# Performance work log

Measured on AMD Instinct MI355X. Metric: run time of the kernel, lower is better.

## Reference

```python
import jax, jax.numpy as jnp
import numpy as np

B, S, D, H, DH = 2, 4096, 1024, 8, 128
BLK, TOPK = 512, 4
NBLK = S // BLK
EPS = 1e-5
NEG = -1e9


def _rope_tables():
    pos = np.arange(S, dtype=np.float32)
    inv = 1.0 / (10000.0 ** (np.arange(0, DH, 2, dtype=np.float32) / DH))
    ang = pos[:, None] * inv[None, :]              # [S, DH/2]
    cos = np.concatenate([np.cos(ang), np.cos(ang)], axis=-1)  # [S, DH]
    sin = np.concatenate([np.sin(ang), np.sin(ang)], axis=-1)
    return jnp.asarray(cos), jnp.asarray(sin)


def setup_inputs() -> dict:
    key = jax.random.key(0)
    ks = jax.random.split(key, 8)
    sc = 0.02
    cos, sin = _rope_tables()
    return {
        "hidden_states": jax.random.normal(ks[0], (B, S, D), jnp.float32),
        "ln1_w": jnp.ones((D,), jnp.float32), "ln1_b": jnp.zeros((D,), jnp.float32),
        "wq": jax.random.normal(ks[1], (D, D), jnp.float32) * sc, "bq": jnp.zeros((D,), jnp.float32),
        "wk": jax.random.normal(ks[2], (D, D), jnp.float32) * sc, "bk": jnp.zeros((D,), jnp.float32),
        "wv": jax.random.normal(ks[3], (D, D), jnp.float32) * sc, "bv": jnp.zeros((D,), jnp.float32),
        "wo": jax.random.normal(ks[4], (D, D), jnp.float32) * sc, "bo": jnp.zeros((D,), jnp.float32),
        "ln2_w": jnp.ones((D,), jnp.float32), "ln2_b": jnp.zeros((D,), jnp.float32),
        "wi": jax.random.normal(ks[5], (D, 4 * D), jnp.float32) * sc, "bi": jnp.zeros((4 * D,), jnp.float32),
        "wo2": jax.random.normal(ks[6], (4 * D, D), jnp.float32) * sc, "bo2": jnp.zeros((D,), jnp.float32),
        "cos": cos, "sin": sin,
    }


def _ln(x, w, b):
    mu = x.mean(-1, keepdims=True)
    var = ((x - mu) ** 2).mean(-1, keepdims=True)
    return (x - mu) * jax.lax.rsqrt(var + EPS) * w + b


def _rotate_half(x):
    x1, x2 = jnp.split(x, 2, axis=-1)
    return jnp.concatenate([-x2, x1], axis=-1)


def _moba_attn(x, wq, bq, wk, bk, wv, bv, wo, bo, cos, sin):
    # projections -> [B, H, S, DH]
    def heads(t):
        return t.reshape(B, S, H, DH).transpose(0, 2, 1, 3)
    q = heads(x @ wq + bq)
    k = heads(x @ wk + bk)
    v = heads(x @ wv + bv)
    c = cos[None, None]; s = sin[None, None]
    q = q * c + _rotate_half(q) * s
    k = k * c + _rotate_half(k) * s
    scale = 1.0 / jnp.sqrt(jnp.asarray(DH, q.dtype))

    # block routing: mean-pooled keys per block -> gate scores [B,H,S,NBLK]
    kmean = k.reshape(B, H, NBLK, BLK, DH).mean(axis=3)
    gate = jnp.einsum("bhsd,bhnd->bhsn", q, kmean) * scale
    pos = jnp.arange(S)
    blk_start = jnp.arange(NBLK) * BLK
    visible = blk_start[None, :] <= pos[:, None]            # [S, NBLK] block has >=1 causal key
    gate = jnp.where(visible[None, None], gate, NEG)
    _, top_idx = jax.lax.top_k(gate, TOPK)                  # [B,H,S,TOPK]
    sel = jax.nn.one_hot(top_idx, NBLK, dtype=jnp.float32).sum(-2)  # [B,H,S,NBLK]
    cur = jax.nn.one_hot(pos // BLK, NBLK, dtype=jnp.float32)       # always attend own block
    sel_blocks = (sel + cur[None, None]) > 0
    sel_keys = jnp.repeat(sel_blocks, BLK, axis=-1)          # [B,H,S,S]

    scores = jnp.einsum("bhid,bhjd->bhij", q, k) * scale
    causal = pos[None, :] <= pos[:, None]
    mask = sel_keys & causal[None, None]
    scores = jnp.where(mask, scores, NEG)
    probs = jax.nn.softmax(scores, axis=-1)
    out = jnp.einsum("bhij,bhjd->bhid", probs, v)
    out = out.transpose(0, 2, 1, 3).reshape(B, S, D)
    return out @ wo + bo


def reference(hidden_states, ln1_w, ln1_b, wq, bq, wk, bk, wv, bv, wo, bo,
              ln2_w, ln2_b, wi, bi, wo2, bo2, cos, sin):
    residual = hidden_states
    x = _ln(hidden_states, ln1_w, ln1_b)
    x = residual + _moba_attn(x, wq, bq, wk, bk, wv, bv, wo, bo, cos, sin)
    residual = x
    h = _ln(x, ln2_w, ln2_b)
    h = jax.nn.gelu(h @ wi + bi, approximate=False)
    h = h @ wo2 + bo2
    return residual + h
```

## Files before the change

### kernel.cpp

```cpp
#include <hip/hip_runtime.h>
#include <cstdint>

#define S_LEN 4096
#define NHEAD 8
#define DHEAD 128
#define DMODEL 1024
#define MOBA_TOPK 4

typedef __attribute__((ext_vector_type(8))) short short8;
typedef __attribute__((ext_vector_type(4))) float f32x4;

__device__ inline float bf2f(short s) {
  return __builtin_bit_cast(float, (unsigned)((unsigned short)s) << 16);
}
__device__ inline short f2bf(float f) {
  unsigned u = __builtin_bit_cast(unsigned, f);
  unsigned r = (u + 0x7fffu + ((u >> 16) & 1u)) >> 16;
  return (short)(unsigned short)r;
}
__device__ inline float toF(float v) { return v; }
__device__ inline float toF(short v) { return bf2f(v); }

#define MFMA(a, b, c) __builtin_amdgcn_mfma_f32_16x16x32_bf16(a, b, c, 0, 0, 0)
#define GLOAD_LDS(gsrc, ldst)                                                  \
  __builtin_amdgcn_global_load_lds(                                            \
      (const __attribute__((address_space(1))) void*)(gsrc),                   \
      (__attribute__((address_space(3))) void*)(ldst), 16, 0, 0)

template <typename T>
__global__ __launch_bounds__(256) void transpose_bf16(const T* __restrict__ in,
                                                      short* __restrict__ out,
                                                      int R, int C) {
  __shared__ float tile[32][33];
  size_t bo = (size_t)blockIdx.z * R * C;
  int c0 = blockIdx.x * 32, r0 = blockIdx.y * 32;
  int tx = threadIdx.x & 31, ty = threadIdx.x >> 5;
#pragma unroll
  for (int i = 0; i < 32; i += 8)
    tile[ty + i][tx] = toF(in[bo + (size_t)(r0 + ty + i) * C + c0 + tx]);
  __syncthreads();
#pragma unroll
  for (int i = 0; i < 32; i += 8)
    out[bo + (size_t)(c0 + ty + i) * R + r0 + tx] = f2bf(tile[tx][ty + i]);
}

__global__ __launch_bounds__(256) void pack_bias(const float* __restrict__ bq,
                                                 const float* __restrict__ bk,
                                                 const float* __restrict__ bv,
                                                 float* __restrict__ dst) {
  int i = blockIdx.x * 256 + threadIdx.x;
  const float* src = (i < 1024) ? bq : (i < 2048) ? bk : bv;
  dst[i] = src[i & 1023];
}

__global__ __launch_bounds__(256) void ln_kernel(const float* __restrict__ x,
                                                 const float* __restrict__ w,
                                                 const float* __restrict__ b,
                                                 short* __restrict__ out) {
  int row = blockIdx.x * 4 + (threadIdx.x >> 6);
  int lane = threadIdx.x & 63;
  const float* xr = x + (size_t)row * DMODEL + lane * 16;
  f32x4 v[4];
  float sum = 0.f, sq = 0.f;
#pragma unroll
  for (int i = 0; i < 4; ++i) {
    v[i] = *(const f32x4*)(xr + i * 4);
#pragma unroll
    for (int j = 0; j < 4; ++j) {
      sum += v[i][j];
      sq += v[i][j] * v[i][j];
    }
  }
#pragma unroll
  for (int d = 1; d < 64; d <<= 1) {
    sum += __shfl_xor(sum, d, 64);
    sq += __shfl_xor(sq, d, 64);
  }
  float mu = sum * (1.f / DMODEL);
  float var = sq * (1.f / DMODEL) - mu * mu;
  float rstd = rsqrtf(var + 1e-5f);
  short* orow = out + (size_t)row * DMODEL;
#pragma unroll
  for (int i = 0; i < 4; ++i)
#pragma unroll
    for (int j = 0; j < 4; ++j) {
      int c = lane * 16 + i * 4 + j;
      orow[c] = f2bf((v[i][j] - mu) * rstd * w[c] + b[c]);
    }
}

template <int BN, int WM, int MODE>
__global__ __launch_bounds__(512, 2) void gemm256(const short* __restrict__ A,
                                                  const short* __restrict__ BT,
                                                  const float* __restrict__ bias,
                                                  const float* __restrict__ residF,
                                                  short* __restrict__ outB,
                                                  float* outF, int M, int N,
                                                  int K) {
  constexpr int MF = 16 / WM;
  constexpr int NWN = 8 / WM;
  constexpr int RB = BN / 64;
  __shared__ alignas(16) short As[2][16384];
  __shared__ alignas(16) short Bs[2][BN * 64];

  const int t = threadIdx.x, lane = t & 63, w = t >> 6;
  const int wm = w / NWN, wn = w % NWN;
  const int m0 = blockIdx.y * 256, n0 = blockIdx.x * BN;
  const int wmBase = wm * (256 / WM);
  const int wnBase = wn * 64;
  const int lr = lane & 15;
  const int koff0 = ((((lane >> 4) << 4)) ^ ((lane & 7) << 4)) >> 1;
  const int koff1 = ((64 + ((lane >> 4) << 4)) ^ ((lane & 7) << 4)) >> 1;

  const f32x4 fz = {0.f, 0.f, 0.f, 0.f};
  f32x4 acc[MF][4];
#pragma unroll
  for (int i = 0; i < MF; ++i)
#pragma unroll
    for (int j = 0; j < 4; ++j) acc[i][j] = fz;

  auto stageA = [&](short* dst, int k0) {
#pragma unroll
    for (int rd = 0; rd < 4; ++rd) {
      int p = (t << 4) + (rd << 13);
      int row = p >> 7;
      int ks = ((p & 127) ^ ((row & 7) << 4)) >> 1;
      GLOAD_LDS(A + (size_t)(m0 + row) * K + k0 + ks, dst + (p >> 1));
    }
  };
  auto stageB = [&](short* dst, int k0) {
#pragma unroll
    for (int rd = 0; rd < RB; ++rd) {
      int p = (t << 4) + (rd << 13);
      int row = p >> 7;
      int ks = ((p & 127) ^ ((row & 7) << 4)) >> 1;
      GLOAD_LDS(BT + (size_t)(n0 + row) * K + k0 + ks, dst + (p >> 1));
    }
  };

  const int NT = K >> 6;
  stageA(&As[0][0], 0);
  stageB(&Bs[0][0], 0);
  __syncthreads();

  for (int kt = 0; kt < NT; ++kt) {
    const int cur = kt & 1;
    if (kt + 1 < NT) {
      stageA(&As[cur ^ 1][0], (kt + 1) << 6);
      stageB(&Bs[cur ^ 1][0], (kt + 1) << 6);
    }
    __builtin_amdgcn_sched_barrier(0);
    short8 bfr[4][2];
#pragma unroll
    for (int ni = 0; ni < 4; ++ni) {
      int rb = (wnBase + ni * 16 + lr) << 6;
      bfr[ni][0] = *(const short8*)(&Bs[cur][rb + koff0]);
      bfr[ni][1] = *(const short8*)(&Bs[cur][rb + koff1]);
    }
#pragma unroll
    for (int pp = 0; pp < MF / 2; ++pp) {
      const int ra0 = (wmBase + (pp * 2) * 16 + lr) << 6;
      const int ra1 = (wmBase + (pp * 2 + 1) * 16 + lr) << 6;
      short8 a00 = *(const short8*)(&As[cur][ra0 + koff0]);
      short8 a01 = *(const short8*)(&As[cur][ra0 + koff1]);
      short8 a10 = *(const short8*)(&As[cur][ra1 + koff0]);
      short8 a11 = *(const short8*)(&As[cur][ra1 + koff1]);
      __builtin_amdgcn_sched_barrier(0);
      __builtin_amdgcn_s_setprio(1);
#pragma unroll
      for (int ni = 0; ni < 4; ++ni) {
        acc[pp * 2][ni] = MFMA(a00, bfr[ni][0], acc[pp * 2][ni]);
        acc[pp * 2][ni] = MFMA(a01, bfr[ni][1], acc[pp * 2][ni]);
        acc[pp * 2 + 1][ni] = MFMA(a10, bfr[ni][0], acc[pp * 2 + 1][ni]);
        acc[pp * 2 + 1][ni] = MFMA(a11, bfr[ni][1], acc[pp * 2 + 1][ni]);
      }
      __builtin_amdgcn_s_setprio(0);
      __builtin_amdgcn_sched_barrier(0);
    }
    __syncthreads();
  }

  const int er = lane >> 4, ec = lane & 15;
#pragma unroll
  for (int mi = 0; mi < MF; ++mi) {
#pragma unroll
    for (int ni = 0; ni < 4; ++ni) {
      int col = n0 + wnBase + ni * 16 + ec;
      float bs = bias[col];
#pragma unroll
      for (int r = 0; r < 4; ++r) {
        int row = m0 + wmBase + mi * 16 + er * 4 + r;
        float v = acc[mi][ni][r] + bs;
        size_t idx = (size_t)row * N + col;
        if (MODE == 1) {
          v += residF[idx];
          outF[idx] = v;
        } else if (MODE == 2) {
          float gl = 0.5f * v * (1.f + erff(v * 0.70710678118654752f));
          outB[idx] = f2bf(gl);
        } else if (MODE == 3) {
          v += outF[idx];
          outF[idx] = v;
        } else {
          int b = row >> 12, s = row & 4095;
          int tens = col >> 10, rem = col & 1023;
          int h = rem >> 7, dh = rem & 127;
          outB[(size_t)tens * 8388608 +
               ((size_t)((b * NHEAD + h) * S_LEN + s)) * DHEAD + dh] = f2bf(v);
        }
      }
    }
  }
}

__global__ __launch_bounds__(256) void rope_kernel(short* __restrict__ q,
                                                   short* __restrict__ k,
                                                   const float* __restrict__ cosT,
                                                   const float* __restrict__ sinT) {
  int row = blockIdx.x * 4 + (threadIdx.x >> 6);
  int lane = threadIdx.x & 63;
  int s = row & (S_LEN - 1);
  float c1 = cosT[s * DHEAD + lane], s1 = sinT[s * DHEAD + lane];
  float c2 = cosT[s * DHEAD + 64 + lane], s2 = sinT[s * DHEAD + 64 + lane];
  size_t base = (size_t)row * DHEAD;
  float a = bf2f(q[base + lane]), bb = bf2f(q[base + 64 + lane]);
  q[base + lane] = f2bf(a * c1 - bb * s1);
  q[base + 64 + lane] = f2bf(bb * c2 + a * s2);
  a = bf2f(k[base + lane]);
  bb = bf2f(k[base + 64 + lane]);
  k[base + lane] = f2bf(a * c1 - bb * s1);
  k[base + 64 + lane] = f2bf(bb * c2 + a * s2);
}

__global__ __launch_bounds__(256) void kmean_kernel(const short* __restrict__ K,
                                                    float* __restrict__ kmean) {
  int n = blockIdx.x, bh = blockIdx.y;
  int t = threadIdx.x;
  int d = t & 127, half = t >> 7;
  const short* base = K + ((size_t)bh * S_LEN + n * 512 + half * 256) * DHEAD + d;
  float s = 0.f;
  for (int i = 0; i < 256; ++i) s += bf2f(base[(size_t)i * DHEAD]);
  __shared__ float red[256];
  red[t] = s;
  __syncthreads();
  if (t < 128)
    kmean[((size_t)bh * 8 + n) * DHEAD + d] = (red[t] + red[t + 128]) * (1.f / 512.f);
}

__global__ __launch_bounds__(256) void gate_kernel(const short* __restrict__ Q,
                                                   const float* __restrict__ kmean,
                                                   unsigned* __restrict__ selmask) {
  int bh = blockIdx.x >> 4;
  int s = ((blockIdx.x & 15) << 8) + threadIdx.x;
  __shared__ float km[8 * DHEAD];
  for (int i = threadIdx.x; i < 8 * DHEAD; i += 256)
    km[i] = kmean[(size_t)bh * 8 * DHEAD + i];
  __syncthreads();
  const short* qrow = Q + ((size_t)bh * S_LEN + s) * DHEAD;
  float g[8] = {0, 0, 0, 0, 0, 0, 0, 0};
  for (int c = 0; c < 16; ++c) {
    short8 qv = *(const short8*)(qrow + c * 8);
    float qf[8];
#pragma unroll
    for (int j = 0; j < 8; ++j) qf[j] = bf2f(qv[j]);
#pragma unroll
    for (int n = 0; n < 8; ++n) {
      float a = 0.f;
#pragma unroll
      for (int j = 0; j < 8; ++j) a += qf[j] * km[n * DHEAD + c * 8 + j];
      g[n] += a;
    }
  }
  int own = s >> 9;
  int nvis = own + 1;
  int kcnt = nvis < MOBA_TOPK ? nvis : MOBA_TOPK;
  unsigned used = 0;
  for (int it = 0; it < kcnt; ++it) {
    float best = -1e38f;
    int bi = 0;
    for (int n = 0; n < nvis; ++n)
      if (!((used >> n) & 1) && g[n] > best) {
        best = g[n];
        bi = n;
      }
    used |= 1u << bi;
  }
  selmask[(size_t)bh * S_LEN + s] = used | (1u << own);
}

__global__ __launch_bounds__(512, 4) void attn_kernel(
    const short* __restrict__ Q, const short* __restrict__ K,
    const short* __restrict__ VT, const unsigned* __restrict__ selmask,
    short* __restrict__ out) {
  const int t = threadIdx.x, lane = t & 63, w = t >> 6;
  const int er = lane >> 4, ec = lane & 15;
  const int er4 = er << 2;

  __shared__ alignas(16) short kbuf[2][8192];
  __shared__ alignas(16) short vbuf[8192];
  __shared__ alignas(16) short plds[8][1152];
  __shared__ unsigned selS[128];
  __shared__ unsigned umS[2];
  __shared__ int kbsS[66];

  const float C = 0.12751742946f;

  for (int pass = 0; pass < 2; ++pass) {
    const int u = pass ? (511 - (int)blockIdx.x) : (int)blockIdx.x;
    const int qt = u & 31, bh = u >> 5;
    const int b = bh >> 3, h = bh & 7;
    const int q0t = qt << 7;

    if (t < 128) selS[t] = selmask[(size_t)bh * S_LEN + q0t + t];
    __syncthreads();
    if (w < 2) {
      unsigned v = selS[w * 64 + lane];
#pragma unroll
      for (int d = 1; d < 64; d <<= 1) v |= __shfl_xor(v, d, 64);
      if (lane == 0) umS[w] = v;
    }
    __syncthreads();
    if (t == 0) {
      unsigned um = umS[0] | umS[1];
      int qmax = q0t + 127;
      int maxb = qmax >> 9;
      int n = 0;
      for (int kb = 0; kb <= maxb; ++kb)
        if ((um >> kb) & 1) {
          int subs = (kb == maxb) ? (((qmax - (kb << 9)) >> 6) + 1) : 8;
          for (int s2 = 0; s2 < subs; ++s2) kbsS[n++] = (kb << 9) + (s2 << 6);
        }
      kbsS[64] = n;
    }
    __syncthreads();
    const int nIter = kbsS[64];

    const size_t sbh = (size_t)bh * S_LEN * DHEAD;
    const short* Kg = K + sbh;
    const short* Vg = VT + (size_t)bh * DHEAD * S_LEN;

    auto kstage = [&](short* dst, int key0) {
#pragma unroll
      for (int rnd = 0; rnd < 2; ++rnd) {
        int p = (t + rnd * 512) << 4;
        int key = p >> 8;
        int lin = p ^ ((key & 7) << 4);
        GLOAD_LDS(Kg + (size_t)(key0 + key) * DHEAD + ((lin & 255) >> 1),
                  dst + (p >> 1));
      }
    };
    auto vstage = [&](int key0) {
#pragma unroll
      for (int rnd = 0; rnd < 2; ++rnd) {
        int p = (t + rnd * 512) << 4;
        int dh = p >> 7;
        int lin = p ^ ((dh & 7) << 4);
        GLOAD_LDS(Vg + (size_t)dh * S_LEN + key0 + ((lin & 127) >> 1),
                  vbuf + (p >> 1));
      }
    };

    const int q0w = q0t + w * 16;
    short8 qf[4];
#pragma unroll
    for (int ks = 0; ks < 4; ++ks)
      qf[ks] = *(const short8*)(Q + sbh + (size_t)(q0w + ec) * DHEAD + ks * 32 + er * 8);

    const unsigned selq = selS[w * 16 + ec];
    const int qmine = q0w + ec;

    const f32x4 fz = {0.f, 0.f, 0.f, 0.f};
    f32x4 oacc[8];
#pragma unroll
    for (int n = 0; n < 8; ++n) oacc[n] = fz;
    float m = -1e30f, lrow = 0.f;
    short* pl = &plds[w][0];

    kstage(&kbuf[0][0], kbsS[0]);
    int cur = 0;
    for (int it = 0; it < nIter; ++it) {
      const int key0 = kbsS[it];
      const int kb = key0 >> 9;
      const int key0n = kbsS[(it + 1 < nIter) ? it + 1 : it];
      vstage(key0);
      kstage(&kbuf[cur ^ 1][0], key0n);
      asm volatile("s_waitcnt vmcnt(4)" ::: "memory");
      __builtin_amdgcn_sched_barrier(0);
      __builtin_amdgcn_s_barrier();
      __builtin_amdgcn_sched_barrier(0);

      const short* kl = &kbuf[cur][0];
      float s[16];
#pragma unroll
      for (int kh = 0; kh < 4; ++kh) {
        short8 kf[4];
#pragma unroll
        for (int ks = 0; ks < 4; ++ks) {
          int slot = ((ks << 2) + er) ^ (ec & 7);
          kf[ks] = *(const short8*)(kl + (((kh << 4) + ec) << 7) + (slot << 3));
        }
        f32x4 a = fz;
#pragma unroll
        for (int ks = 0; ks < 4; ++ks) a = MFMA(kf[ks], qf[ks], a);
#pragma unroll
        for (int r = 0; r < 4; ++r) s[kh * 4 + r] = a[r];
      }

      int kqoff = qmine - key0 - er4;
      if (!((selq >> kb) & 1)) kqoff = -1;
      float mx = -1e30f;
#pragma unroll
      for (int kh = 0; kh < 4; ++kh)
#pragma unroll
        for (int r = 0; r < 4; ++r)
          mx = fmaxf(mx, ((kh * 16 + r) <= kqoff) ? s[kh * 4 + r] : -1e30f);
      mx = fmaxf(mx, __shfl_xor(mx, 16, 64));
      mx = fmaxf(mx, __shfl_xor(mx, 32, 64));

      if (__any(mx > m + 62.0f)) {
        float mnew = fmaxf(m, mx);
        float corr = __builtin_amdgcn_exp2f((m - mnew) * C);
        m = mnew;
        lrow *= corr;
        float c0 = __shfl(corr, er4 + 0, 16);
        float c1 = __shfl(corr, er4 + 1, 16);
        float c2 = __shfl(corr, er4 + 2, 16);
        float c3 = __shfl(corr, er4 + 3, 16);
#pragma unroll
        for (int n = 0; n < 8; ++n) {
          oacc[n][0] *= c0;
          oacc[n][1] *= c1;
          oacc[n][2] *= c2;
          oacc[n][3] *= c3;
        }
      }

      const float mc = m * C;
      float e[16];
      float rs = 0.f;
#pragma unroll
      for (int kh = 0; kh < 4; ++kh)
#pragma unroll
        for (int r = 0; r < 4; ++r) {
          int i = kh * 4 + r;
          float ex = __builtin_amdgcn_exp2f(fmaf(s[i], C, -mc));
          ex = ((kh * 16 + r) <= kqoff) ? ex : 0.f;
          e[i] = ex;
          rs += ex;
        }
      rs += __shfl_xor(rs, 16, 64);
      rs += __shfl_xor(rs, 32, 64);
      lrow += rs;

      short* pb = pl + ec * 72 + er4;
#pragma unroll
      for (int kh = 0; kh < 4; ++kh) {
        unsigned u0, u1;
        asm("v_cvt_pk_bf16_f32 %0, %1, %2"
            : "=v"(u0) : "v"(e[kh * 4 + 0]), "v"(e[kh * 4 + 1]));
        asm("v_cvt_pk_bf16_f32 %0, %1, %2"
            : "=v"(u1) : "v"(e[kh * 4 + 2]), "v"(e[kh * 4 + 3]));
        *(unsigned*)(pb + kh * 16) = u0;
        *(unsigned*)(pb + kh * 16 + 2) = u1;
      }
      asm volatile("s_waitcnt lgkmcnt(0)" ::: "memory");
      __builtin_amdgcn_sched_barrier(0);
      const short8 pa0 = *(const short8*)(pl + ec * 72 + er * 8);
      const short8 pa1 = *(const short8*)(pl + ec * 72 + 32 + er * 8);

      asm volatile("s_waitcnt vmcnt(2)" ::: "memory");
      __builtin_amdgcn_sched_barrier(0);
      __builtin_amdgcn_s_barrier();
      __builtin_amdgcn_sched_barrier(0);

#pragma unroll
      for (int kc = 0; kc < 2; ++kc) {
        const short8 pa = kc ? pa1 : pa0;
#pragma unroll
        for (int n = 0; n < 8; ++n) {
          int slot = ((kc << 2) + er) ^ (ec & 7);
          short8 vf = *(const short8*)(vbuf + (((n << 4) + ec) << 6) + (slot << 3));
          oacc[n] = MFMA(pa, vf, oacc[n]);
        }
      }
      __builtin_amdgcn_sched_barrier(0);
      __builtin_amdgcn_s_barrier();
      __builtin_amdgcn_sched_barrier(0);
      cur ^= 1;
    }

    float rl[4];
#pragma unroll
    for (int r = 0; r < 4; ++r) rl[r] = 1.0f / __shfl(lrow, er4 + r, 16);
#pragma unroll
    for (int n = 0; n < 8; ++n) {
#pragma unroll
      for (int r = 0; r < 4; ++r) {
        float v = oacc[n][r] * rl[r];
        out[((size_t)(b * S_LEN + q0w + er4 + r)) * DMODEL + h * DHEAD + n * 16 + ec] = f2bf(v);
      }
    }
    asm volatile("s_waitcnt vmcnt(0)" ::: "memory");
    __syncthreads();
  }
}

extern "C" void kernel_launch(void* const* d_in, const int* in_sizes, int n_in,
                              void* d_out, int out_size, void* d_ws,
                              size_t ws_size, hipStream_t stream) {
  (void)in_sizes; (void)n_in; (void)out_size; (void)ws_size;
  const float* hidden = (const float*)d_in[0];
  const float* ln1w = (const float*)d_in[1];
  const float* ln1b = (const float*)d_in[2];
  const float* wq = (const float*)d_in[3];
  const float* bq = (const float*)d_in[4];
  const float* wk = (const float*)d_in[5];
  const float* bk = (const float*)d_in[6];
  const float* wv = (const float*)d_in[7];
  const float* bv = (const float*)d_in[8];
  const float* wo = (const float*)d_in[9];
  const float* bo = (const float*)d_in[10];
  const float* ln2w = (const float*)d_in[11];
  const float* ln2b = (const float*)d_in[12];
  const float* wi = (const float*)d_in[13];
  const float* bi = (const float*)d_in[14];
  const float* wo2 = (const float*)d_in[15];
  const float* bo2 = (const float*)d_in[16];
  const float* cosT = (const float*)d_in[17];
  const float* sinT = (const float*)d_in[18];
  float* outF = (float*)d_out;

  char* base = (char*)d_ws;
  size_t off = 0;
  auto alloc = [&](size_t bytes) {
    char* p = base + off;
    off = (off + bytes + 255) & ~(size_t)255;
    return p;
  };
  short* wqkvT = (short*)alloc((size_t)3072 * 1024 * 2);
  short* woT = (short*)alloc((size_t)1024 * 1024 * 2);
  short* wiT = (short*)alloc((size_t)4096 * 1024 * 2);
  short* wo2T = (short*)alloc((size_t)1024 * 4096 * 2);
  float* biasC = (float*)alloc((size_t)3072 * 4);
  float* kmeanB = (float*)alloc((size_t)16 * 8 * 128 * 4);
  unsigned* selm = (unsigned*)alloc((size_t)16 * 4096 * 4);
  short* xattn = (short*)alloc((size_t)8192 * 1024 * 2);
  short* h2 = (short*)alloc((size_t)8192 * 1024 * 2);
  size_t phase = off;
  short* xln = (short*)alloc((size_t)8192 * 1024 * 2);
  short* qb = (short*)alloc((size_t)16 * 4096 * 128 * 2);
  short* kb = (short*)alloc((size_t)16 * 4096 * 128 * 2);
  short* vb = (short*)alloc((size_t)16 * 4096 * 128 * 2);
  short* vT = (short*)alloc((size_t)16 * 128 * 4096 * 2);
  short* g = (short*)(base + phase);

  dim3 T256(256);
  dim3 T512(512);
  transpose_bf16<float><<<dim3(32, 32, 1), T256, 0, stream>>>(wq, wqkvT, 1024, 1024);
  transpose_bf16<float><<<dim3(32, 32, 1), T256, 0, stream>>>(wk, wqkvT + 1048576, 1024, 1024);
  transpose_bf16<float><<<dim3(32, 32, 1), T256, 0, stream>>>(wv, wqkvT + 2097152, 1024, 1024);
  transpose_bf16<float><<<dim3(32, 32, 1), T256, 0, stream>>>(wo, woT, 1024, 1024);
  transpose_bf16<float><<<dim3(128, 32, 1), T256, 0, stream>>>(wi, wiT, 1024, 4096);
  transpose_bf16<float><<<dim3(32, 128, 1), T256, 0, stream>>>(wo2, wo2T, 4096, 1024);
  pack_bias<<<12, T256, 0, stream>>>(bq, bk, bv, biasC);

  ln_kernel<<<2048, T256, 0, stream>>>(hidden, ln1w, ln1b, xln);

  gemm256<256, 2, 4><<<dim3(12, 32), T512, 0, stream>>>(xln, wqkvT, biasC, nullptr, qb, nullptr, 8192, 3072, 1024);

  rope_kernel<<<16384, T256, 0, stream>>>(qb, kb, cosT, sinT);
  transpose_bf16<short><<<dim3(4, 128, 16), T256, 0, stream>>>(vb, vT, 4096, 128);

  kmean_kernel<<<dim3(8, 16), T256, 0, stream>>>(kb, kmeanB);
  gate_kernel<<<256, T256, 0, stream>>>(qb, kmeanB, selm);

  attn_kernel<<<dim3(256), T512, 0, stream>>>(qb, kb, vT, selm, xattn);

  gemm256<128, 4, 1><<<dim3(8, 32), T512, 0, stream>>>(xattn, woT, bo, hidden, nullptr, outF, 8192, 1024, 1024);
  ln_kernel<<<2048, T256, 0, stream>>>(outF, ln2w, ln2b, h2);
  gemm256<256, 2, 2><<<dim3(16, 32), T512, 0, stream>>>(h2, wiT, bi, nullptr, g, nullptr, 8192, 4096, 1024);
  gemm256<128, 4, 3><<<dim3(8, 32), T512, 0, stream>>>(g, wo2T, bo2, nullptr, nullptr, outF, 8192, 1024, 4096);
}
```

Before: 675.0 us.

## Merge prep and rope/V-transpose launches, remap GEMM blocks, split attention grid

Folds the six weight transposes and the bias pack into one prep kernel, and the RoPE and V transpose into one kernel, so fewer kernels are launched. GEMM block indices are permuted so that consecutive block IDs are spread across eight chunks, presumably to balance work or cache use across XCDs. The QKV GEMM moves from BN=256 to BN=128 tiles, doubling its grid. Attention now launches 512 blocks, one tile each, instead of 256 blocks looping over two paired tiles. This gives better occupancy and scheduling flexibility, at the cost of per-block setup overhead.

Result: faster. 642.5 us (-4.8%).

```diff
diff --git a/kernel.cpp b/kernel.cpp
--- a/kernel.cpp
+++ b/kernel.cpp
@@ -18,8 +18,6 @@
   unsigned r = (u + 0x7fffu + ((u >> 16) & 1u)) >> 16;
   return (short)(unsigned short)r;
 }
-__device__ inline float toF(float v) { return v; }
-__device__ inline float toF(short v) { return bf2f(v); }
 
 #define MFMA(a, b, c) __builtin_amdgcn_mfma_f32_16x16x32_bf16(a, b, c, 0, 0, 0)
 #define GLOAD_LDS(gsrc, ldst)                                                  \
@@ -27,30 +25,50 @@
       (const __attribute__((address_space(1))) void*)(gsrc),                   \
       (__attribute__((address_space(3))) void*)(ldst), 16, 0, 0)
 
-template <typename T>
-__global__ __launch_bounds__(256) void transpose_bf16(const T* __restrict__ in,
-                                                      short* __restrict__ out,
-                                                      int R, int C) {
+__global__ __launch_bounds__(256) void prep_kernel(
+    const float* __restrict__ wq, const float* __restrict__ wk,
+    const float* __restrict__ wv, const float* __restrict__ wo,
+    const float* __restrict__ wi, const float* __restrict__ wo2,
+    const float* __restrict__ bq, const float* __restrict__ bk,
+    const float* __restrict__ bv, short* __restrict__ wqkvT,
+    short* __restrict__ woT, short* __restrict__ wiT,
+    short* __restrict__ wo2T, float* __restrict__ biasC) {
   __shared__ float tile[32][33];
-  size_t bo = (size_t)blockIdx.z * R * C;
-  int c0 = blockIdx.x * 32, r0 = blockIdx.y * 32;
-  int tx = threadIdx.x & 31, ty = threadIdx.x >> 5;
+  const int b = blockIdx.x;
+  const int tx = threadIdx.x & 31, ty = threadIdx.x >> 5;
+  const float* in;
+  short* out;
+  int R, C, bx, by;
+  if (b < 3072) {
+    int seg = b >> 10, idx = b & 1023;
+    in = seg == 0 ? wq : seg == 1 ? wk : wv;
+    out = wqkvT + seg * 1048576;
+    R = 1024; C = 1024; bx = idx & 31; by = idx >> 5;
+  } else if (b < 4096) {
+    int idx = b - 3072;
+    in = wo; out = woT; R = 1024; C = 1024; bx = idx & 31; by = idx >> 5;
+  } else if (b < 8192) {
+    int idx = b - 4096;
+    in = wi; out = wiT; R = 1024; C = 4096; bx = idx & 127; by = idx >> 7;
+  } else if (b < 12288) {
+    int idx = b - 8192;
+    in = wo2; out = wo2T; R = 4096; C = 1024; bx = idx & 31; by = idx >> 5;
+  } else {
+    int i = (b - 12288) * 256 + threadIdx.x;
+    if (i < 3072) {
+      const float* src = (i < 1024) ? bq : (i < 2048) ? bk : bv;
+      biasC[i] = src[i & 1023];
+    }
+    return;
+  }
+  int c0 = bx * 32, r0 = by * 32;
 #pragma unroll
   for (int i = 0; i < 32; i += 8)
-    tile[ty + i][tx] = toF(in[bo + (size_t)(r0 + ty + i) * C + c0 + tx]);
+    tile[ty + i][tx] = in[(size_t)(r0 + ty + i) * C + c0 + tx];
   __syncthreads();
 #pragma unroll
   for (int i = 0; i < 32; i += 8)
-    out[bo + (size_t)(c0 + ty + i) * R + r0 + tx] = f2bf(tile[tx][ty + i]);
-}
-
-__global__ __launch_bounds__(256) void pack_bias(const float* __restrict__ bq,
-                                                 const float* __restrict__ bk,
-                                                 const float* __restrict__ bv,
-                                                 float* __restrict__ dst) {
-  int i = blockIdx.x * 256 + threadIdx.x;
-  const float* src = (i < 1024) ? bq : (i < 2048) ? bk : bv;
-  dst[i] = src[i & 1023];
+    out[(size_t)(c0 + ty + i) * R + r0 + tx] = f2bf(tile[tx][ty + i]);
 }
 
 __global__ __launch_bounds__(256) void ln_kernel(const float* __restrict__ x,
@@ -105,7 +123,10 @@
 
   const int t = threadIdx.x, lane = t & 63, w = t >> 6;
   const int wm = w / NWN, wn = w % NWN;
-  const int m0 = blockIdx.y * 256, n0 = blockIdx.x * BN;
+  int bid = blockIdx.y * gridDim.x + blockIdx.x;
+  const int chunk = (gridDim.x * gridDim.y) >> 3;
+  bid = (bid & 7) * chunk + (bid >> 3);
+  const int m0 = (bid / gridDim.x) * 256, n0 = (bid % gridDim.x) * BN;
   const int wmBase = wm * (256 / WM);
   const int wnBase = wn * 64;
   const int lr = lane & 15;
@@ -213,23 +234,41 @@
   }
 }
 
-__global__ __launch_bounds__(256) void rope_kernel(short* __restrict__ q,
-                                                   short* __restrict__ k,
-                                                   const float* __restrict__ cosT,
-                                                   const float* __restrict__ sinT) {
-  int row = blockIdx.x * 4 + (threadIdx.x >> 6);
-  int lane = threadIdx.x & 63;
-  int s = row & (S_LEN - 1);
-  float c1 = cosT[s * DHEAD + lane], s1 = sinT[s * DHEAD + lane];
-  float c2 = cosT[s * DHEAD + 64 + lane], s2 = sinT[s * DHEAD + 64 + lane];
-  size_t base = (size_t)row * DHEAD;
-  float a = bf2f(q[base + lane]), bb = bf2f(q[base + 64 + lane]);
-  q[base + lane] = f2bf(a * c1 - bb * s1);
-  q[base + 64 + lane] = f2bf(bb * c2 + a * s2);
-  a = bf2f(k[base + lane]);
-  bb = bf2f(k[base + 64 + lane]);
-  k[base + lane] = f2bf(a * c1 - bb * s1);
-  k[base + 64 + lane] = f2bf(bb * c2 + a * s2);
+__global__ __launch_bounds__(256) void ropevt_kernel(
+    short* __restrict__ q, short* __restrict__ k,
+    const short* __restrict__ vb, short* __restrict__ vT,
+    const float* __restrict__ cosT, const float* __restrict__ sinT) {
+  __shared__ float tile[32][33];
+  const int b = blockIdx.x;
+  if (b < 16384) {
+    int row = b * 4 + (threadIdx.x >> 6);
+    int lane = threadIdx.x & 63;
+    int s = row & (S_LEN - 1);
+    float c1 = cosT[s * DHEAD + lane], s1 = sinT[s * DHEAD + lane];
+    float c2 = cosT[s * DHEAD + 64 + lane], s2 = sinT[s * DHEAD + 64 + lane];
+    size_t base = (size_t)row * DHEAD;
+    float a = bf2f(q[base + lane]), bb = bf2f(q[base + 64 + lane]);
+    q[base + lane] = f2bf(a * c1 - bb * s1);
+    q[base + 64 + lane] = f2bf(bb * c2 + a * s2);
+    a = bf2f(k[base + lane]);
+    bb = bf2f(k[base + 64 + lane]);
+    k[base + lane] = f2bf(a * c1 - bb * s1);
+    k[base + 64 + lane] = f2bf(bb * c2 + a * s2);
+    return;
+  }
+  int idx = b - 16384;
+  int bz = idx >> 9, rem = idx & 511;
+  int bx = rem & 3, by = rem >> 2;
+  size_t bo = (size_t)bz * S_LEN * DHEAD;
+  int c0 = bx * 32, r0 = by * 32;
+  int tx = threadIdx.x & 31, ty = threadIdx.x >> 5;
+#pragma unroll
+  for (int i = 0; i < 32; i += 8)
+    tile[ty + i][tx] = bf2f(vb[bo + (size_t)(r0 + ty + i) * DHEAD + c0 + tx]);
+  __syncthreads();
+#pragma unroll
+  for (int i = 0; i < 32; i += 8)
+    vT[bo + (size_t)(c0 + ty + i) * S_LEN + r0 + tx] = f2bf(tile[tx][ty + i]);
 }
 
 __global__ __launch_bounds__(256) void kmean_kernel(const short* __restrict__ K,
@@ -305,204 +344,202 @@
 
   const float C = 0.12751742946f;
 
-  for (int pass = 0; pass < 2; ++pass) {
-    const int u = pass ? (511 - (int)blockIdx.x) : (int)blockIdx.x;
-    const int qt = u & 31, bh = u >> 5;
-    const int b = bh >> 3, h = bh & 7;
-    const int q0t = qt << 7;
-
-    if (t < 128) selS[t] = selmask[(size_t)bh * S_LEN + q0t + t];
-    __syncthreads();
-    if (w < 2) {
-      unsigned v = selS[w * 64 + lane];
-#pragma unroll
-      for (int d = 1; d < 64; d <<= 1) v |= __shfl_xor(v, d, 64);
-      if (lane == 0) umS[w] = v;
-    }
-    __syncthreads();
-    if (t == 0) {
-      unsigned um = umS[0] | umS[1];
-      int qmax = q0t + 127;
-      int maxb = qmax >> 9;
-      int n = 0;
-      for (int kb = 0; kb <= maxb; ++kb)
-        if ((um >> kb) & 1) {
-          int subs = (kb == maxb) ? (((qmax - (kb << 9)) >> 6) + 1) : 8;
-          for (int s2 = 0; s2 < subs; ++s2) kbsS[n++] = (kb << 9) + (s2 << 6);
-        }
-      kbsS[64] = n;
-    }
-    __syncthreads();
-    const int nIter = kbsS[64];
-
-    const size_t sbh = (size_t)bh * S_LEN * DHEAD;
-    const short* Kg = K + sbh;
-    const short* Vg = VT + (size_t)bh * DHEAD * S_LEN;
-
-    auto kstage = [&](short* dst, int key0) {
-#pragma unroll
-      for (int rnd = 0; rnd < 2; ++rnd) {
-        int p = (t + rnd * 512) << 4;
-        int key = p >> 8;
-        int lin = p ^ ((key & 7) << 4);
-        GLOAD_LDS(Kg + (size_t)(key0 + key) * DHEAD + ((lin & 255) >> 1),
-                  dst + (p >> 1));
-      }
-    };
-    auto vstage = [&](int key0) {
-#pragma unroll
-      for (int rnd = 0; rnd < 2; ++rnd) {
-        int p = (t + rnd * 512) << 4;
-        int dh = p >> 7;
-        int lin = p ^ ((dh & 7) << 4);
-        GLOAD_LDS(Vg + (size_t)dh * S_LEN + key0 + ((lin & 127) >> 1),
-                  vbuf + (p >> 1));
-      }
-    };
-
-    const int q0w = q0t + w * 16;
-    short8 qf[4];
-#pragma unroll
-    for (int ks = 0; ks < 4; ++ks)
-      qf[ks] = *(const short8*)(Q + sbh + (size_t)(q0w + ec) * DHEAD + ks * 32 + er * 8);
-
-    const unsigned selq = selS[w * 16 + ec];
-    const int qmine = q0w + ec;
-
-    const f32x4 fz = {0.f, 0.f, 0.f, 0.f};
-    f32x4 oacc[8];
-#pragma unroll
-    for (int n = 0; n < 8; ++n) oacc[n] = fz;
-    float m = -1e30f, lrow = 0.f;
-    short* pl = &plds[w][0];
-
-    kstage(&kbuf[0][0], kbsS[0]);
-    int cur = 0;
-    for (int it = 0; it < nIter; ++it) {
-      const int key0 = kbsS[it];
-      const int kb = key0 >> 9;
-      const int key0n = kbsS[(it + 1 < nIter) ? it + 1 : it];
-      vstage(key0);
-      kstage(&kbuf[cur ^ 1][0], key0n);
-      asm volatile("s_waitcnt vmcnt(4)" ::: "memory");
-      __builtin_amdgcn_sched_barrier(0);
-      __builtin_amdgcn_s_barrier();
-      __builtin_amdgcn_sched_barrier(0);
-
-      const short* kl = &kbuf[cur][0];
-      float s[16];
-#pragma unroll
-      for (int kh = 0; kh < 4; ++kh) {
-        short8 kf[4];
-#pragma unroll
-        for (int ks = 0; ks < 4; ++ks) {
-          int slot = ((ks << 2) + er) ^ (ec & 7);
-          kf[ks] = *(const short8*)(kl + (((kh << 4) + ec) << 7) + (slot << 3));
-        }
-        f32x4 a = fz;
-#pragma unroll
-        for (int ks = 0; ks < 4; ++ks) a = MFMA(kf[ks], qf[ks], a);
-#pragma unroll
-        for (int r = 0; r < 4; ++r) s[kh * 4 + r] = a[r];
-      }
-
-      int kqoff = qmine - key0 - er4;
-      if (!((selq >> kb) & 1)) kqoff = -1;
-      float mx = -1e30f;
-#pragma unroll
-      for (int kh = 0; kh < 4; ++kh)
-#pragma unroll
-        for (int r = 0; r < 4; ++r)
-          mx = fmaxf(mx, ((kh * 16 + r) <= kqoff) ? s[kh * 4 + r] : -1e30f);
-      mx = fmaxf(mx, __shfl_xor(mx, 16, 64));
-      mx = fmaxf(mx, __shfl_xor(mx, 32, 64));
-
-      if (__any(mx > m + 62.0f)) {
-        float mnew = fmaxf(m, mx);
-        float corr = __builtin_amdgcn_exp2f((m - mnew) * C);
-        m = mnew;
-        lrow *= corr;
-        float c0 = __shfl(corr, er4 + 0, 16);
-        float c1 = __shfl(corr, er4 + 1, 16);
-        float c2 = __shfl(corr, er4 + 2, 16);
-        float c3 = __shfl(corr, er4 + 3, 16);
-#pragma unroll
-        for (int n = 0; n < 8; ++n) {
-          oacc[n][0] *= c0;
-          oacc[n][1] *= c1;
-          oacc[n][2] *= c2;
-          oacc[n][3] *= c3;
-        }
-      }
-
-      const float mc = m * C;
-      float e[16];
-      float rs = 0.f;
-#pragma unroll
-      for (int kh = 0; kh < 4; ++kh)
-#pragma unroll
-        for (int r = 0; r < 4; ++r) {
-          int i = kh * 4 + r;
-          float ex = __builtin_amdgcn_exp2f(fmaf(s[i], C, -mc));
-          ex = ((kh * 16 + r) <= kqoff) ? ex : 0.f;
-          e[i] = ex;
-          rs += ex;
-        }
-      rs += __shfl_xor(rs, 16, 64);
-      rs += __shfl_xor(rs, 32, 64);
-      lrow += rs;
-
-      short* pb = pl + ec * 72 + er4;
-#pragma unroll
-      for (int kh = 0; kh < 4; ++kh) {
-        unsigned u0, u1;
-        asm("v_cvt_pk_bf16_f32 %0, %1, %2"
-            : "=v"(u0) : "v"(e[kh * 4 + 0]), "v"(e[kh * 4 + 1]));
-        asm("v_cvt_pk_bf16_f32 %0, %1, %2"
-            : "=v"(u1) : "v"(e[kh * 4 + 2]), "v"(e[kh * 4 + 3]));
-        *(unsigned*)(pb + kh * 16) = u0;
-        *(unsigned*)(pb + kh * 16 + 2) = u1;
-      }
-      asm volatile("s_waitcnt lgkmcnt(0)" ::: "memory");
-      __builtin_amdgcn_sched_barrier(0);
-      const short8 pa0 = *(const short8*)(pl + ec * 72 + er * 8);
-      const short8 pa1 = *(const short8*)(pl + ec * 72 + 32 + er * 8);
-
-      asm volatile("s_waitcnt vmcnt(2)" ::: "memory");
-      __builtin_amdgcn_sched_barrier(0);
-      __builtin_amdgcn_s_barrier();
-      __builtin_amdgcn_sched_barrier(0);
-
-#pragma unroll
-      for (int kc = 0; kc < 2; ++kc) {
-        const short8 pa = kc ? pa1 : pa0;
-#pragma unroll
-        for (int n = 0; n < 8; ++n) {
-          int slot = ((kc << 2) + er) ^ (ec & 7);
-          short8 vf = *(const short8*)(vbuf + (((n << 4) + ec) << 6) + (slot << 3));
-          oacc[n] = MFMA(pa, vf, oacc[n]);
-        }
-      }
-      __builtin_amdgcn_sched_barrier(0);
-      __builtin_amdgcn_s_barrier();
-      __builtin_amdgcn_sched_barrier(0);
-      cur ^= 1;
-    }
-
-    float rl[4];
-#pragma unroll
-    for (int r = 0; r < 4; ++r) rl[r] = 1.0f / __shfl(lrow, er4 + r, 16);
-#pragma unroll
-    for (int n = 0; n < 8; ++n) {
+  const int bid = blockIdx.x;
+  const int u = (bid < 256) ? bid : 767 - bid;
+  const int qt = u & 31, bh = u >> 5;
+  const int b = bh >> 3, h = bh & 7;
+  const int q0t = qt << 7;
+
+  if (t < 128) selS[t] = selmask[(size_t)bh * S_LEN + q0t + t];
+  __syncthreads();
+  if (w < 2) {
+    unsigned v = selS[w * 64 + lane];
+#pragma unroll
+    for (int d = 1; d < 64; d <<= 1) v |= __shfl_xor(v, d, 64);
+    if (lane == 0) umS[w] = v;
+  }
+  __syncthreads();
+  if (t == 0) {
+    unsigned um = umS[0] | umS[1];
+    int qmax = q0t + 127;
+    int maxb = qmax >> 9;
+    int n = 0;
+    for (int kb = 0; kb <= maxb; ++kb)
+      if ((um >> kb) & 1) {
+        int subs = (kb == maxb) ? (((qmax - (kb << 9)) >> 6) + 1) : 8;
+        for (int s2 = 0; s2 < subs; ++s2) kbsS[n++] = (kb << 9) + (s2 << 6);
+      }
+    kbsS[64] = n;
+  }
+  __syncthreads();
+  const int nIter = kbsS[64];
+
+  const size_t sbh = (size_t)bh * S_LEN * DHEAD;
+  const short* Kg = K + sbh;
+  const short* Vg = VT + (size_t)bh * DHEAD * S_LEN;
+
+  auto kstage = [&](short* dst, int key0) {
+#pragma unroll
+    for (int rnd = 0; rnd < 2; ++rnd) {
+      int p = (t + rnd * 512) << 4;
+      int key = p >> 8;
+      int lin = p ^ ((key & 7) << 4);
+      GLOAD_LDS(Kg + (size_t)(key0 + key) * DHEAD + ((lin & 255) >> 1),
+                dst + (p >> 1));
+    }
+  };
+  auto vstage = [&](int key0) {
+#pragma unroll
+    for (int rnd = 0; rnd < 2; ++rnd) {
+      int p = (t + rnd * 512) << 4;
+      int dh = p >> 7;
+      int lin = p ^ ((dh & 7) << 4);
+      GLOAD_LDS(Vg + (size_t)dh * S_LEN + key0 + ((lin & 127) >> 1),
+                vbuf + (p >> 1));
+    }
+  };
+
+  const int q0w = q0t + w * 16;
+  short8 qf[4];
+#pragma unroll
+  for (int ks = 0; ks < 4; ++ks)
+    qf[ks] = *(const short8*)(Q + sbh + (size_t)(q0w + ec) * DHEAD + ks * 32 + er * 8);
+
+  const unsigned selq = selS[w * 16 + ec];
+  const int qmine = q0w + ec;
+
+  const f32x4 fz = {0.f, 0.f, 0.f, 0.f};
+  f32x4 oacc[8];
+#pragma unroll
+  for (int n = 0; n < 8; ++n) oacc[n] = fz;
+  float m = -1e30f, lrow = 0.f;
+  short* pl = &plds[w][0];
+
+  kstage(&kbuf[0][0], kbsS[0]);
+  int cur = 0;
+  for (int it = 0; it < nIter; ++it) {
+    const int key0 = kbsS[it];
+    const int kb = key0 >> 9;
+    const int key0n = kbsS[(it + 1 < nIter) ? it + 1 : it];
+    vstage(key0);
+    kstage(&kbuf[cur ^ 1][0], key0n);
+    asm volatile("s_waitcnt vmcnt(4)" ::: "memory");
+    __builtin_amdgcn_sched_barrier(0);
+    __builtin_amdgcn_s_barrier();
+    __builtin_amdgcn_sched_barrier(0);
+
+    const short* kl = &kbuf[cur][0];
+    float s[16];
+#pragma unroll
+    for (int kh = 0; kh < 4; ++kh) {
+      short8 kf[4];
+#pragma unroll
+      for (int ks = 0; ks < 4; ++ks) {
+        int slot = ((ks << 2) + er) ^ (ec & 7);
+        kf[ks] = *(const short8*)(kl + (((kh << 4) + ec) << 7) + (slot << 3));
+      }
+      f32x4 a = fz;
+#pragma unroll
+      for (int ks = 0; ks < 4; ++ks) a = MFMA(kf[ks], qf[ks], a);
+#pragma unroll
+      for (int r = 0; r < 4; ++r) s[kh * 4 + r] = a[r];
+    }
+
+    int kqoff = qmine - key0 - er4;
+    if (!((selq >> kb) & 1)) kqoff = -1;
+    float mx = -1e30f;
+#pragma unroll
+    for (int kh = 0; kh < 4; ++kh)
+#pragma unroll
+      for (int r = 0; r < 4; ++r)
+        mx = fmaxf(mx, ((kh * 16 + r) <= kqoff) ? s[kh * 4 + r] : -1e30f);
+    mx = fmaxf(mx, __shfl_xor(mx, 16, 64));
+    mx = fmaxf(mx, __shfl_xor(mx, 32, 64));
+
+    if (__any(mx > m + 62.0f)) {
+      float mnew = fmaxf(m, mx);
+      float corr = __builtin_amdgcn_exp2f((m - mnew) * C);
+      m = mnew;
+      lrow *= corr;
+      float c0 = __shfl(corr, er4 + 0, 16);
+      float c1 = __shfl(corr, er4 + 1, 16);
+      float c2 = __shfl(corr, er4 + 2, 16);
+      float c3 = __shfl(corr, er4 + 3, 16);
+#pragma unroll
+      for (int n = 0; n < 8; ++n) {
+        oacc[n][0] *= c0;
+        oacc[n][1] *= c1;
+        oacc[n][2] *= c2;
+        oacc[n][3] *= c3;
+      }
+    }
+
+    const float mc = m * C;
+    float e[16];
+    float rs = 0.f;
+#pragma unroll
+    for (int kh = 0; kh < 4; ++kh)
 #pragma unroll
       for (int r = 0; r < 4; ++r) {
-        float v = oacc[n][r] * rl[r];
-        out[((size_t)(b * S_LEN + q0w + er4 + r)) * DMODEL + h * DHEAD + n * 16 + ec] = f2bf(v);
-      }
-    }
-    asm volatile("s_waitcnt vmcnt(0)" ::: "memory");
-    __syncthreads();
-  }
+        int i = kh * 4 + r;
+        float ex = __builtin_amdgcn_exp2f(fmaf(s[i], C, -mc));
+        ex = ((kh * 16 + r) <= kqoff) ? ex : 0.f;
+        e[i] = ex;
+        rs += ex;
+      }
+    rs += __shfl_xor(rs, 16, 64);
+    rs += __shfl_xor(rs, 32, 64);
+    lrow += rs;
+
+    short* pb = pl + ec * 72 + er4;
+#pragma unroll
+    for (int kh = 0; kh < 4; ++kh) {
+      unsigned u0, u1;
+      asm("v_cvt_pk_bf16_f32 %0, %1, %2"
+          : "=v"(u0) : "v"(e[kh * 4 + 0]), "v"(e[kh * 4 + 1]));
+      asm("v_cvt_pk_bf16_f32 %0, %1, %2"
+          : "=v"(u1) : "v"(e[kh * 4 + 2]), "v"(e[kh * 4 + 3]));
+      *(unsigned*)(pb + kh * 16) = u0;
+      *(unsigned*)(pb + kh * 16 + 2) = u1;
+    }
+    asm volatile("s_waitcnt lgkmcnt(0)" ::: "memory");
+    __builtin_amdgcn_sched_barrier(0);
+    const short8 pa0 = *(const short8*)(pl + ec * 72 + er * 8);
+    const short8 pa1 = *(const short8*)(pl + ec * 72 + 32 + er * 8);
+
+    asm volatile("s_waitcnt vmcnt(2)" ::: "memory");
+    __builtin_amdgcn_sched_barrier(0);
+    __builtin_amdgcn_s_barrier();
+    __builtin_amdgcn_sched_barrier(0);
+
+#pragma unroll
+    for (int kc = 0; kc < 2; ++kc) {
+      const short8 pa = kc ? pa1 : pa0;
+#pragma unroll
+      for (int n = 0; n < 8; ++n) {
+        int slot = ((kc << 2) + er) ^ (ec & 7);
+        short8 vf = *(const short8*)(vbuf + (((n << 4) + ec) << 6) + (slot << 3));
+        oacc[n] = MFMA(pa, vf, oacc[n]);
+      }
+    }
+    __builtin_amdgcn_sched_barrier(0);
+    __builtin_amdgcn_s_barrier();
+    __builtin_amdgcn_sched_barrier(0);
+    cur ^= 1;
+  }
+
+  float rl[4];
+#pragma unroll
+  for (int r = 0; r < 4; ++r) rl[r] = 1.0f / __shfl(lrow, er4 + r, 16);
+#pragma unroll
+  for (int n = 0; n < 8; ++n) {
+#pragma unroll
+    for (int r = 0; r < 4; ++r) {
+      float v = oacc[n][r] * rl[r];
+      out[((size_t)(b * S_LEN + q0w + er4 + r)) * DMODEL + h * DHEAD + n * 16 + ec] = f2bf(v);
+    }
+  }
+  asm volatile("s_waitcnt vmcnt(0)" ::: "memory");
 }
 
 extern "C" void kernel_launch(void* const* d_in, const int* in_sizes, int n_in,
@@ -556,25 +593,19 @@
 
   dim3 T256(256);
   dim3 T512(512);
-  transpose_bf16<float><<<dim3(32, 32, 1), T256, 0, stream>>>(wq, wqkvT, 1024, 1024);
-  transpose_bf16<float><<<dim3(32, 32, 1), T256, 0, stream>>>(wk, wqkvT + 1048576, 1024, 1024);
-  transpose_bf16<float><<<dim3(32, 32, 1), T256, 0, stream>>>(wv, wqkvT + 2097152, 1024, 1024);
-  transpose_bf16<float><<<dim3(32, 32, 1), T256, 0, stream>>>(wo, woT, 1024, 1024);
-  transpose_bf16<float><<<dim3(128, 32, 1), T256, 0, stream>>>(wi, wiT, 1024, 4096);
-  transpose_bf16<float><<<dim3(32, 128, 1), T256, 0, stream>>>(wo2, wo2T, 4096, 1024);
-  pack_bias<<<12, T256, 0, stream>>>(bq, bk, bv, biasC);
+  prep_kernel<<<12301, T256, 0, stream>>>(wq, wk, wv, wo, wi, wo2, bq, bk, bv,
+                                          wqkvT, woT, wiT, wo2T, biasC);
 
   ln_kernel<<<2048, T256, 0, stream>>>(hidden, ln1w, ln1b, xln);
 
-  gemm256<256, 2, 4><<<dim3(12, 32), T512, 0, stream>>>(xln, wqkvT, biasC, nullptr, qb, nullptr, 8192, 3072, 1024);
-
-  rope_kernel<<<16384, T256, 0, stream>>>(qb, kb, cosT, sinT);
-  transpose_bf16<short><<<dim3(4, 128, 16), T256, 0, stream>>>(vb, vT, 4096, 128);
+  gemm256<128, 4, 4><<<dim3(24, 32), T512, 0, stream>>>(xln, wqkvT, biasC, nullptr, qb, nullptr, 8192, 3072, 1024);
+
+  ropevt_kernel<<<24576, T256, 0, stream>>>(qb, kb, vb, vT, cosT, sinT);
 
   kmean_kernel<<<dim3(8, 16), T256, 0, stream>>>(kb, kmeanB);
   gate_kernel<<<256, T256, 0, stream>>>(qb, kmeanB, selm);
 
-  attn_kernel<<<dim3(256), T512, 0, stream>>>(qb, kb, vT, selm, xattn);
+  attn_kernel<<<dim3(512), T512, 0, stream>>>(qb, kb, vT, selm, xattn);
 
   gemm256<128, 4, 1><<<dim3(8, 32), T512, 0, stream>>>(xattn, woT, bo, hidden, nullptr, outF, 8192, 1024, 1024);
   ln_kernel<<<2048, T256, 0, stream>>>(outF, ln2w, ln2b, h2);
```
